# Kernel tuning notes

Hardware: AMD Instinct MI355X
Metric: run time of the kernel (lower is better)

The kernel has to match this reference:

```python
import jax, jax.numpy as jnp
import numpy as np

NEG = -1e30  # log-space 'zero' that keeps gradients finite (vs -inf)


def setup_inputs() -> dict:
    key = jax.random.key(0)
    k1, k2, k3, k4 = jax.random.split(key, 4)
    B, T, V, S = 32, 2048, 128, 256
    predictions = jax.random.normal(k1, (B, T, V), dtype=jnp.float32)
    # input lengths in [T//2, T]; target lengths in [S//4, S]; labels in [1, V) (0 is blank)
    prediction_lengths = jax.random.randint(k2, (B,), T // 2, T + 1, dtype=jnp.int32)
    ground_truths = jax.random.randint(k3, (B, S), 1, V, dtype=jnp.int32)
    ground_truth_lengths = jax.random.randint(k4, (B,), S // 4, S + 1, dtype=jnp.int32)
    return {
        "predictions": predictions,
        "prediction_lengths": prediction_lengths,
        "ground_truths": ground_truths,
        "ground_truth_lengths": ground_truth_lengths,
    }


def _ctc_loss(log_probs, targets, input_lengths, target_lengths, blank=0):
    # log_probs: [T, B, V]; targets: [B, S]
    T, B, V = log_probs.shape
    S = targets.shape[1]
    L = 2 * S + 1  # extended label sequence: blank, l1, blank, l2, ..., blank
    ext = jnp.full((B, L), blank, dtype=targets.dtype).at[:, 1::2].set(targets)
    # skip transition s-2 -> s allowed iff ext[s] != blank and ext[s] != ext[s-2]
    skip = jnp.concatenate(
        [jnp.zeros((B, 2), dtype=bool), (ext[:, 2:] != blank) & (ext[:, 2:] != ext[:, :-2])],
        axis=1,
    )
    # gather per-extended-label log-probs: [T, B, L]
    lp_ext = jnp.take_along_axis(log_probs, jnp.broadcast_to(ext[None], (T, B, L)), axis=2)

    alpha0 = (
        jnp.full((B, L), NEG, dtype=log_probs.dtype)
        .at[:, 0].set(lp_ext[0, :, 0])
        .at[:, 1].set(lp_ext[0, :, 1])
    )

    def step(alpha, lp_t):
        a1 = alpha
        a2 = jnp.pad(alpha[:, :-1], ((0, 0), (1, 0)), constant_values=NEG)
        a3 = jnp.where(skip, jnp.pad(alpha[:, :-2], ((0, 0), (2, 0)), constant_values=NEG), NEG)
        m = jnp.maximum(jnp.maximum(a1, a2), a3)
        new = m + jnp.log(jnp.exp(a1 - m) + jnp.exp(a2 - m) + jnp.exp(a3 - m)) + lp_t
        return new, new

    _, alphas = jax.lax.scan(step, alpha0, lp_ext[1:])
    alphas = jnp.concatenate([alpha0[None], alphas], axis=0)  # [T, B, L]

    bidx = jnp.arange(B)
    alpha_final = alphas[input_lengths - 1, bidx]  # [B, L] at each sequence's last frame
    last = 2 * target_lengths  # index of final blank; last-1 is final label
    loss = -jnp.logaddexp(alpha_final[bidx, last], alpha_final[bidx, last - 1])
    loss = jnp.where(loss < 1e10, loss, 0.0)  # zero_infinity=True
    # torch reduction='mean': per-sample loss / target_length, then batch mean
    return (loss / target_lengths.astype(loss.dtype)).mean()


def reference(predictions, prediction_lengths, ground_truths, ground_truth_lengths):
    # module: transpose to [T, B, V], log_softmax over vocab, then CTC loss
    log_probs = jax.nn.log_softmax(jnp.transpose(predictions, (1, 0, 2)), axis=2)
    return _ctc_loss(log_probs, ground_truths, prediction_lengths, ground_truth_lengths, blank=0)
```

## Files before the change

kernel.cpp:

```cpp
#include <hip/hip_runtime.h>
#include <math.h>

constexpr int V = 128;

__device__ __forceinline__ double dpp_shr1_f64(double x) {
    int lo = __builtin_amdgcn_update_dpp(0, __double2loint(x), 0x138, 0xf, 0xf, false);
    int hi = __builtin_amdgcn_update_dpp(0, __double2hiint(x), 0x138, 0xf, 0xf, false);
    return __hiloint2double(hi, lo);
}
__device__ __forceinline__ double dpp_shl1_f64(double x) {
    int lo = __builtin_amdgcn_update_dpp(0, __double2loint(x), 0x130, 0xf, 0xf, false);
    int hi = __builtin_amdgcn_update_dpp(0, __double2hiint(x), 0x130, 0xf, 0xf, false);
    return __hiloint2double(hi, lo);
}

__global__ __launch_bounds__(256) void ctc_prelude(
    const float* __restrict__ pred, const int* __restrict__ gt,
    const int* __restrict__ gt_len, const int* __restrict__ pred_len,
    float* __restrict__ g, float* __restrict__ z, float* __restrict__ x0a,
    int T, int S)
{
    int wid  = blockIdx.x * 4 + (threadIdx.x >> 6);
    int lane = threadIdx.x & 63;
    int w4   = threadIdx.x >> 6;
    int b    = wid / T;
    int t    = wid - b * T;
    if (t >= pred_len[b]) return;
    __shared__ float rows[4][V];

    const float2* p = (const float2*)pred + (size_t)wid * 64;
    float2 v = p[lane];
    rows[w4][2 * lane]     = v.x;
    rows[w4][2 * lane + 1] = v.y;
    float x0 = __shfl(v.x, 0, 64);
    float s = __expf(v.x) + __expf(v.y);
    #pragma unroll
    for (int off = 32; off >= 1; off >>= 1) s += __shfl_xor(s, off, 64);
    if (lane == 0) { z[wid] = __logf(s); x0a[wid] = v.x; }

    int4 la = *(const int4*)(gt + b * S + 4 * lane);
    int tl = gt_len[b];
    float4 o;
    o.x = (4 * lane + 0 < tl) ? __expf(rows[w4][la.x] - x0) : 0.f;
    o.y = (4 * lane + 1 < tl) ? __expf(rows[w4][la.y] - x0) : 0.f;
    o.z = (4 * lane + 2 < tl) ? __expf(rows[w4][la.z] - x0) : 0.f;
    o.w = (4 * lane + 3 < tl) ? __expf(rows[w4][la.w] - x0) : 0.f;
    *(float4*)(g + (size_t)wid * 256 + 4 * lane) = o;
}

__global__ __launch_bounds__(64) void ctc_scan_bi(
    const float* __restrict__ g,
    const int*   __restrict__ pred_len,
    const int*   __restrict__ gt,
    const int*   __restrict__ gt_len,
    const float* __restrict__ z,
    const float* __restrict__ x0a,
    double*      __restrict__ fwdv,
    double*      __restrict__ bwdv,
    int*         __restrict__ Kf,
    int*         __restrict__ Kb,
    int* done, int* gdone, float* lossb,
    float* __restrict__ out,
    int T, int S, int B)
{
    const int blk  = blockIdx.x;
    const int b    = blk >> 1;
    const int dir  = blk & 1;
    const int lane = threadIdx.x;
    const int len  = pred_len[b];
    const int tl   = gt_len[b];
    const int L    = 2 * tl + 1;
    const int m    = (len + 1) >> 1;

    int4 la = *(const int4*)(gt + b * S + 4 * lane);
    int law_up = __shfl_up(la.w, 1, 64);
    int lax_dn = __shfl_down(la.x, 1, 64);
    const double sk0 = (lane > 0 && la.x != law_up) ? 1.0 : 0.0;
    const double sk1 = (la.y != la.x) ? 1.0 : 0.0;
    const double sk2 = (la.z != la.y) ? 1.0 : 0.0;
    const double sk3 = (la.w != la.z) ? 1.0 : 0.0;
    const double sk4 = (lax_dn != la.w) ? 1.0 : 0.0;

    const char* gb = (const char*)(g + (size_t)b * T * 256) + lane * 16;

    float4 raw[16];
    double u[9];
    int K = 0;

    auto RESCALE = [&]() {
        double mx = u[0];
        #pragma unroll
        for (int j = 1; j < 9; ++j) mx = fmax(mx, u[j]);
        #pragma unroll
        for (int off = 32; off >= 1; off >>= 1)
            mx = fmax(mx, __shfl_xor(mx, off, 64));
        int k = ((__double2hiint(mx) >> 20) & 0x7ff) - 1023;
        #pragma unroll
        for (int j = 0; j < 9; ++j) u[j] = ldexp(u[j], -k);
        K += k;
    };

    if (dir == 0) {
        #pragma unroll
        for (int i = 0; i < 16; ++i)
            raw[i] = *(const float4*)(gb + (size_t)i * 1024);
        #pragma unroll
        for (int j = 0; j < 9; ++j) u[j] = 0.0;
        if (lane == 0) { u[0] = 1.0; u[1] = (double)raw[0].x; }
        raw[0] = *(const float4*)(gb + (size_t)16 * 1024);
        const char* pf = gb + (size_t)17 * 1024;

        auto FSTEP = [&](int i) {
            float4 g4 = raw[i];
            raw[i] = *(const float4*)pf; pf += 1024;
            double um1 = dpp_shr1_f64(u[7]);
            double gx = (double)g4.x, gy = (double)g4.y;
            double gz = (double)g4.z, gw = (double)g4.w;
            u[8] = u[8] + u[7];
            u[7] = (fma(sk3, u[5], u[6]) + u[7]) * gw;
            u[6] = u[6] + u[5];
            u[5] = (fma(sk2, u[3], u[4]) + u[5]) * gz;
            u[4] = u[4] + u[3];
            u[3] = (fma(sk1, u[1], u[2]) + u[3]) * gy;
            u[2] = u[2] + u[1];
            u[1] = (fma(sk0, um1, u[0]) + u[1]) * gx;
            u[0] = u[0] + um1;
        };

        #pragma unroll
        for (int t = 1; t < 16; ++t) FSTEP(t);
        int tb = 16;
        for (; tb + 16 <= m; tb += 16) {
            #pragma unroll
            for (int i = 0; i < 16; ++i) FSTEP(i);
            if (((tb + 16) & 63) == 0) RESCALE();
        }
        #pragma unroll
        for (int i = 0; i < 15; ++i)
            if (tb + i < m) FSTEP(i);
        RESCALE();

        double* outv = fwdv + (size_t)b * 520;
        #pragma unroll
        for (int j = 0; j < 8; ++j) outv[8 * lane + j] = u[j];
        if (lane == 63) outv[512] = u[8];
        if (lane == 0)  Kf[b] = K;
    } else {
        const int nb = len - m;
        #pragma unroll
        for (int i = 0; i < 16; ++i)
            raw[i] = *(const float4*)(gb + (size_t)(len - 1 - i) * 1024);
        #pragma unroll
        for (int j = 0; j < 8; ++j) {
            int s = 8 * lane + j;
            u[j] = (s == 2 * tl || s == 2 * tl - 1) ? 1.0 : 0.0;
        }
        u[8] = (L == 513) ? 1.0 : 0.0;
        const char* pf = gb + (size_t)(len - 17) * 1024;

        auto BSTEP = [&](int i) {
            float4 g4 = raw[i];
            raw[i] = *(const float4*)pf; pf -= 1024;
            double d0 = dpp_shl1_f64(u[0]);
            if (lane == 63) d0 = u[8];
            double p1 = (double)g4.x * u[1], p3 = (double)g4.y * u[3];
            double p5 = (double)g4.z * u[5], p7 = (double)g4.w * u[7];
            double dp = dpp_shl1_f64(p1);
            u[0] = u[0] + p1;
            u[1] = fma(sk1, p3, u[2]) + p1;
            u[2] = u[2] + p3;
            u[3] = fma(sk2, p5, u[4]) + p3;
            u[4] = u[4] + p5;
            u[5] = fma(sk3, p7, u[6]) + p5;
            u[6] = u[6] + p7;
            u[7] = fma(sk4, dp, d0) + p7;
        };

        #pragma unroll
        for (int k = 0; k < 16; ++k) BSTEP(k);
        int kb = 16;
        for (; kb + 16 <= nb; kb += 16) {
            #pragma unroll
            for (int i = 0; i < 16; ++i) BSTEP(i);
            if (((kb + 16) & 63) == 0) RESCALE();
        }
        #pragma unroll
        for (int i = 0; i < 15; ++i)
            if (kb + i < nb) BSTEP(i);
        RESCALE();

        double* outv = bwdv + (size_t)b * 520;
        #pragma unroll
        for (int j = 0; j < 8; ++j) outv[8 * lane + j] = u[j];
        if (lane == 63) outv[512] = u[8];
        if (lane == 0)  Kb[b] = K;
    }

    __threadfence();
    int prev = 0;
    if (lane == 0)
        prev = __hip_atomic_fetch_add(&done[b], 1, __ATOMIC_ACQ_REL,
                                      __HIP_MEMORY_SCOPE_AGENT);
    prev = __shfl(prev, 0, 64);
    if (prev == 0) return;
    __threadfence();

    const double* f = fwdv + (size_t)b * 520;
    const double* w = bwdv + (size_t)b * 520;
    double c = 0.0;
    #pragma unroll
    for (int j = 0; j < 8; ++j)
        c = fma(f[8 * lane + j], w[8 * lane + j], c);
    if (lane == 63) c = fma(f[512], w[512], c);
    #pragma unroll
    for (int off = 32; off >= 1; off >>= 1) c += __shfl_xor(c, off, 64);

    double zs = 0.0;
    for (int t = lane; t < len; t += 64)
        zs += (double)z[b * T + t] - (double)x0a[b * T + t];
    #pragma unroll
    for (int off = 32; off >= 1; off >>= 1) zs += __shfl_xor(zs, off, 64);

    if (lane == 0) {
        double logp = log(c)
                    + (double)(Kf[b] + Kb[b]) * 0.6931471805599453 - zs;
        double loss = -logp;
        if (!(loss < 1e10)) loss = 0.0;
        lossb[b] = (float)(loss / (double)tl);
        __threadfence();
        int pg = __hip_atomic_fetch_add(gdone, 1, __ATOMIC_ACQ_REL,
                                        __HIP_MEMORY_SCOPE_AGENT);
        if (pg == B - 1) {
            __threadfence();
            float ssum = 0.0f;
            for (int i = 0; i < B; ++i) ssum += lossb[i];
            out[0] = ssum / (float)B;
        }
    }
}

constexpr int SPL  = 9;
constexpr int RING = 32;

__global__ void ctc_reduce_kernel(const float* __restrict__ ls,
                                  float* __restrict__ out, int B)
{
    if (blockIdx.x == 0 && threadIdx.x == 0) {
        float s = 0.0f;
        for (int i = 0; i < B; ++i) s += ls[i];
        out[0] = s / (float)B;
    }
}

__global__ __launch_bounds__(256) void softmax_z_kernel(
    const float* __restrict__ pred, float* __restrict__ z, int nrows)
{
    int w    = blockIdx.x * 4 + (threadIdx.x >> 6);
    int lane = threadIdx.x & 63;
    if (w >= nrows) return;
    const float2* p = (const float2*)pred;
    float2 v = p[(size_t)w * 64 + lane];
    float s = __expf(v.x) + __expf(v.y);
    #pragma unroll
    for (int off = 32; off >= 1; off >>= 1) s += __shfl_xor(s, off, 64);
    if (lane == 0) z[w] = __logf(s);
}

__device__ __forceinline__ void ctc_step_fb(
    const float* __restrict__ rowbase, const int* __restrict__ goff,
    const double* __restrict__ skd, double (&u)[SPL], int lane)
{
    float gf[SPL];
    #pragma unroll
    for (int j = 0; j < SPL; ++j)
        gf[j] = *(const float*)((const char*)rowbase + goff[j]);
    double um1 = __shfl_up(u[8], 1, 64);
    double um2 = __shfl_up(u[7], 1, 64);
    if (lane == 0) { um1 = 0.0; um2 = 0.0; }
    #pragma unroll
    for (int jj = 0; jj < SPL; ++jj) {
        int j = SPL - 1 - jj;
        double a2 = (j >= 1) ? u[j - 1] : um1;
        double a3 = (j >= 2) ? u[j - 2] : ((j == 1) ? um1 : um2);
        double t  = fma(skd[j], a3, a2) + u[j];
        u[j] = t * (double)gf[j];
    }
}

__device__ __forceinline__ void ctc_rescale_fb(double (&u)[SPL], int& K)
{
    double m = u[0];
    #pragma unroll
    for (int j = 1; j < SPL; ++j) m = fmax(m, u[j]);
    #pragma unroll
    for (int off = 32; off >= 1; off >>= 1) m = fmax(m, __shfl_xor(m, off, 64));
    if (m > 0.0) {
        int e = (__double2hiint(m) >> 20) & 0x7ff;
        int k = e - 1023;
        #pragma unroll
        for (int j = 0; j < SPL; ++j) u[j] = ldexp(u[j], -k);
        K += k;
    }
}

__global__ __launch_bounds__(64) void ctc_scan_kernel(
    const float* __restrict__ pred, const int* __restrict__ pred_len,
    const int* __restrict__ gt, const int* __restrict__ gt_len,
    const float* __restrict__ z, float* __restrict__ loss_out, int T, int S)
{
    const int b    = blockIdx.x;
    const int lane = threadIdx.x;
    const int len  = pred_len[b];
    const int tl   = gt_len[b];
    const int L    = 2 * tl + 1;

    __shared__ float ring[RING][V];
    __shared__ int   gts[512];

    for (int i = lane; i < S; i += 64) gts[i] = gt[b * S + i];
    __syncthreads();

    int    goff[SPL];
    double skd[SPL];
    #pragma unroll
    for (int j = 0; j < SPL; ++j) {
        int s = SPL * lane + j;
        int e = 0, ep = 0;
        if (s < L && (s & 1)) e = gts[s >> 1];
        if (s >= 2 && s < L && (s & 1)) ep = gts[(s - 2) >> 1];
        goff[j] = e * 4;
        skd[j]  = (s >= 2 && s < L && e != 0 && e != ep) ? 1.0 : 0.0;
    }

    const float2* rowp = (const float2*)(pred + (size_t)b * T * V);
    float2 raw[16];

    #pragma unroll
    for (int i = 0; i < 16; ++i) raw[i] = rowp[(size_t)i * 64 + lane];
    #pragma unroll
    for (int i = 0; i < 16; ++i) {
        float2 w; w.x = __expf(raw[i].x); w.y = __expf(raw[i].y);
        *(float2*)&ring[i][2 * lane] = w;
    }
    #pragma unroll
    for (int i = 0; i < 16; ++i) raw[i] = rowp[(size_t)(16 + i) * 64 + lane];
    #pragma unroll
    for (int i = 0; i < 16; ++i) {
        float2 w; w.x = __expf(raw[i].x); w.y = __expf(raw[i].y);
        *(float2*)&ring[16 + i][2 * lane] = w;
    }
    #pragma unroll
    for (int i = 0; i < 16; ++i) {
        int r = 32 + i; if (r > T - 1) r = T - 1;
        raw[i] = rowp[(size_t)r * 64 + lane];
    }

    double u[SPL];
    #pragma unroll
    for (int j = 0; j < SPL; ++j) {
        int s = SPL * lane + j;
        float w0 = *(const float*)((const char*)&ring[0][0] + goff[j]);
        u[j] = (s < 2) ? (double)w0 : 0.0;
    }
    int K = 0;

    for (int t = 1; t < 16 && t < len; ++t)
        ctc_step_fb(&ring[t & (RING - 1)][0], goff, skd, u, lane);
    ctc_rescale_fb(u, K);

    int tb = 16;
    for (; tb + 16 <= len; tb += 16) {
        #pragma unroll
        for (int i = 0; i < 16; ++i) {
            float2 w; w.x = __expf(raw[i].x); w.y = __expf(raw[i].y);
            *(float2*)&ring[(tb + 16 + i) & (RING - 1)][2 * lane] = w;
        }
        #pragma unroll
        for (int i = 0; i < 16; ++i) {
            int r = tb + 32 + i; if (r > T - 1) r = T - 1;
            raw[i] = rowp[(size_t)r * 64 + lane];
        }
        #pragma unroll
        for (int i = 0; i < 16; ++i)
            ctc_step_fb(&ring[(tb + i) & (RING - 1)][0], goff, skd, u, lane);
        ctc_rescale_fb(u, K);
    }

    for (int t = tb; t < len; ++t)
        ctc_step_fb(&ring[t & (RING - 1)][0], goff, skd, u, lane);

    double contrib = 0.0;
    #pragma unroll
    for (int j = 0; j < SPL; ++j) {
        int s = SPL * lane + j;
        if (s == L - 1 || s == L - 2) contrib += u[j];
    }
    #pragma unroll
    for (int off = 32; off >= 1; off >>= 1)
        contrib += __shfl_xor(contrib, off, 64);

    double zsum = 0.0;
    for (int t = lane; t < len; t += 64) zsum += (double)z[b * T + t];
    #pragma unroll
    for (int off = 32; off >= 1; off >>= 1)
        zsum += __shfl_xor(zsum, off, 64);

    if (lane == 0) {
        double lg    = log(contrib);
        double alpha = lg + (double)K * 0.6931471805599453 - zsum;
        double loss  = -alpha;
        if (!(loss < 1e10)) loss = 0.0;
        loss_out[b] = (float)(loss / (double)tl);
    }
}

extern "C" void kernel_launch(void* const* d_in, const int* in_sizes, int n_in,
                              void* d_out, int out_size, void* d_ws, size_t ws_size,
                              hipStream_t stream) {
    const float* pred = (const float*)d_in[0];
    const int*   plen = (const int*)d_in[1];
    const int*   gts  = (const int*)d_in[2];
    const int*   glen = (const int*)d_in[3];

    const int B = in_sizes[1];
    const int S = in_sizes[2] / B;
    const int T = in_sizes[0] / (B * V);
    const size_t BT = (size_t)B * T;

    float* out = (float*)d_out;
    char*  ws  = (char*)d_ws;

    size_t off_fl  = 0;
    size_t off_z   = 1024;
    size_t off_x0  = off_z   + BT * 4;
    size_t off_fw  = (off_x0 + BT * 4 + 255) & ~(size_t)255;
    size_t off_bw  = off_fw  + (size_t)B * 520 * 8;
    size_t off_kf  = off_bw  + (size_t)B * 520 * 8;
    size_t off_kb  = off_kf  + (size_t)B * 4;
    size_t off_g   = (off_kb + (size_t)B * 4 + 1023) & ~(size_t)1023;
    size_t need    = off_g + BT * 256 * 4;

    bool fast_ok = (ws_size >= need) && (S == 256) && (T % 4 == 0) &&
                   (T >= 96) && (B >= 1) && (B <= 64);

    if (fast_ok) {
        int*    done  = (int*)(ws + off_fl);
        int*    gdone = (int*)(ws + off_fl + 256);
        float*  lossb = (float*)(ws + off_fl + 512);
        float*  zp    = (float*)(ws + off_z);
        float*  x0a   = (float*)(ws + off_x0);
        double* fw    = (double*)(ws + off_fw);
        double* bw    = (double*)(ws + off_bw);
        int*    kf    = (int*)(ws + off_kf);
        int*    kb    = (int*)(ws + off_kb);
        float*  g     = (float*)(ws + off_g);

        hipMemsetAsync(ws + off_fl, 0, 512, stream);
        ctc_prelude<<<B * T / 4, 256, 0, stream>>>(pred, gts, glen, plen,
                                                   g, zp, x0a, T, S);
        ctc_scan_bi<<<2 * B, 64, 0, stream>>>(g, plen, gts, glen, zp, x0a,
                                              fw, bw, kf, kb,
                                              done, gdone, lossb, out, T, S, B);
    } else {
        float* zbuf = (float*)ws;
        float* lb   = zbuf + BT;
        int nrows = B * T;
        softmax_z_kernel<<<(nrows + 3) / 4, 256, 0, stream>>>(pred, zbuf, nrows);
        ctc_scan_kernel<<<B, 64, 0, stream>>>(pred, plen, gts, glen, zbuf, lb, T, S);
        ctc_reduce_kernel<<<1, 64, 0, stream>>>(lb, out, B);
    }
}
```

Before: 174.9 us.

## Switch CTC alpha/beta recurrences from fp64 to fp32 with per-lane exponent scaling

Runs the forward and backward CTC scans in fp32 instead of fp64. Because fp32 has too little range for one shared scale, each lane now keeps its own power-of-two exponent, and neighbouring lanes' exponents are kept within 32 of each other by a DPP-based propagation. Values crossing between lanes are adjusted by a factor, rescaling happens every 8 steps, and the final combine merges per-lane exponents in fp64. This aims to cut fp64 ALU and DPP cost on the serial critical path, but adds rescale work and risks accuracy or underflow problems.

```diff
diff --git a/kernel.cpp b/kernel.cpp
--- a/kernel.cpp
+++ b/kernel.cpp
@@ -3,15 +3,19 @@
 
 constexpr int V = 128;
 
-__device__ __forceinline__ double dpp_shr1_f64(double x) {
-    int lo = __builtin_amdgcn_update_dpp(0, __double2loint(x), 0x138, 0xf, 0xf, false);
-    int hi = __builtin_amdgcn_update_dpp(0, __double2hiint(x), 0x138, 0xf, 0xf, false);
-    return __hiloint2double(hi, lo);
-}
-__device__ __forceinline__ double dpp_shl1_f64(double x) {
-    int lo = __builtin_amdgcn_update_dpp(0, __double2loint(x), 0x130, 0xf, 0xf, false);
-    int hi = __builtin_amdgcn_update_dpp(0, __double2hiint(x), 0x130, 0xf, 0xf, false);
-    return __hiloint2double(hi, lo);
+__device__ __forceinline__ float dpp_shr1_f32(float x) {
+    int v = __builtin_amdgcn_update_dpp(0, __float_as_int(x), 0x138, 0xf, 0xf, false);
+    return __int_as_float(v);
+}
+__device__ __forceinline__ float dpp_shl1_f32(float x) {
+    int v = __builtin_amdgcn_update_dpp(0, __float_as_int(x), 0x130, 0xf, 0xf, false);
+    return __int_as_float(v);
+}
+__device__ __forceinline__ int dpp_shr1_i32(int x) {
+    return __builtin_amdgcn_update_dpp(0, x, 0x138, 0xf, 0xf, false);
+}
+__device__ __forceinline__ int dpp_shl1_i32(int x) {
+    return __builtin_amdgcn_update_dpp(0, x, 0x130, 0xf, 0xf, false);
 }
 
 __global__ __launch_bounds__(256) void ctc_prelude(
@@ -55,10 +59,10 @@
     const int*   __restrict__ gt_len,
     const float* __restrict__ z,
     const float* __restrict__ x0a,
-    double*      __restrict__ fwdv,
-    double*      __restrict__ bwdv,
-    int*         __restrict__ Kf,
-    int*         __restrict__ Kb,
+    float*       __restrict__ fwdv,
+    float*       __restrict__ bwdv,
+    int*         __restrict__ Kfv,
+    int*         __restrict__ Kbv,
     int* done, int* gdone, float* lossb,
     float* __restrict__ out,
     int T, int S, int B)
@@ -75,76 +79,99 @@
     int4 la = *(const int4*)(gt + b * S + 4 * lane);
     int law_up = __shfl_up(la.w, 1, 64);
     int lax_dn = __shfl_down(la.x, 1, 64);
-    const double sk0 = (lane > 0 && la.x != law_up) ? 1.0 : 0.0;
-    const double sk1 = (la.y != la.x) ? 1.0 : 0.0;
-    const double sk2 = (la.z != la.y) ? 1.0 : 0.0;
-    const double sk3 = (la.w != la.z) ? 1.0 : 0.0;
-    const double sk4 = (lax_dn != la.w) ? 1.0 : 0.0;
+    const float sk0 = (lane > 0 && la.x != law_up) ? 1.f : 0.f;
+    const float sk1 = (la.y != la.x) ? 1.f : 0.f;
+    const float sk2 = (la.z != la.y) ? 1.f : 0.f;
+    const float sk3 = (la.w != la.z) ? 1.f : 0.f;
+    const float sk4 = (lax_dn != la.w) ? 1.f : 0.f;
 
     const char* gb = (const char*)(g + (size_t)b * T * 256) + lane * 16;
 
     float4 raw[16];
-    double u[9];
-    int K = 0;
-
-    auto RESCALE = [&]() {
-        double mx = u[0];
-        #pragma unroll
-        for (int j = 1; j < 9; ++j) mx = fmax(mx, u[j]);
-        #pragma unroll
-        for (int off = 32; off >= 1; off >>= 1)
-            mx = fmax(mx, __shfl_xor(mx, off, 64));
-        int k = ((__double2hiint(mx) >> 20) & 0x7ff) - 1023;
-        #pragma unroll
-        for (int j = 0; j < 9; ++j) u[j] = ldexp(u[j], -k);
-        K += k;
-    };
+    float u[9];
+    int   K   = 0;
+    float fac = 1.0f;
 
     if (dir == 0) {
         #pragma unroll
         for (int i = 0; i < 16; ++i)
             raw[i] = *(const float4*)(gb + (size_t)i * 1024);
         #pragma unroll
-        for (int j = 0; j < 9; ++j) u[j] = 0.0;
-        if (lane == 0) { u[0] = 1.0; u[1] = (double)raw[0].x; }
+        for (int j = 0; j < 9; ++j) u[j] = 0.f;
+        if (lane == 0) { u[0] = 1.f; u[1] = raw[0].x; }
         raw[0] = *(const float4*)(gb + (size_t)16 * 1024);
         const char* pf = gb + (size_t)17 * 1024;
+
+        auto RESCALE = [&]() {
+            float mx = u[0];
+            #pragma unroll
+            for (int j = 1; j < 9; ++j) mx = fmaxf(mx, u[j]);
+            bool dead = !(mx > 0.f);
+            int  k = dead ? 0 : ((int)((__float_as_uint(mx) >> 23) & 0xff) - 127);
+            #pragma unroll
+            for (int j = 0; j < 9; ++j) u[j] = ldexpf(u[j], -k);
+            K += k;
+            int K0 = K;
+            int nbrdead = dpp_shr1_i32(dead ? 1 : 0);
+            if (lane == 0) nbrdead = 1;
+            int Kn = 0;
+            #pragma unroll
+            for (int r = 0; r < 16; ++r) {
+                Kn = dpp_shr1_i32(K);
+                int cand = Kn - 32;
+                int Kr = (!dead && !nbrdead && cand > K) ? cand : K;
+                K = dead ? Kn : Kr;
+            }
+            int up = K - K0;
+            if (up > 0) {
+                #pragma unroll
+                for (int j = 0; j < 9; ++j) u[j] = ldexpf(u[j], -up);
+            }
+            int d = Kn - K;
+            d = d < -126 ? -126 : (d > 32 ? 32 : d);
+            fac = ldexpf(1.0f, d);
+        };
 
         auto FSTEP = [&](int i) {
             float4 g4 = raw[i];
             raw[i] = *(const float4*)pf; pf += 1024;
-            double um1 = dpp_shr1_f64(u[7]);
-            double gx = (double)g4.x, gy = (double)g4.y;
-            double gz = (double)g4.z, gw = (double)g4.w;
+            float um1 = dpp_shr1_f32(u[7]) * fac;
             u[8] = u[8] + u[7];
-            u[7] = (fma(sk3, u[5], u[6]) + u[7]) * gw;
+            u[7] = (fmaf(sk3, u[5], u[6]) + u[7]) * g4.w;
             u[6] = u[6] + u[5];
-            u[5] = (fma(sk2, u[3], u[4]) + u[5]) * gz;
+            u[5] = (fmaf(sk2, u[3], u[4]) + u[5]) * g4.z;
             u[4] = u[4] + u[3];
-            u[3] = (fma(sk1, u[1], u[2]) + u[3]) * gy;
+            u[3] = (fmaf(sk1, u[1], u[2]) + u[3]) * g4.y;
             u[2] = u[2] + u[1];
-            u[1] = (fma(sk0, um1, u[0]) + u[1]) * gx;
+            u[1] = (fmaf(sk0, um1, u[0]) + u[1]) * g4.x;
             u[0] = u[0] + um1;
         };
 
         #pragma unroll
-        for (int t = 1; t < 16; ++t) FSTEP(t);
+        for (int t = 1; t < 16; ++t) {
+            FSTEP(t);
+            if (t == 7 || t == 15) RESCALE();
+        }
         int tb = 16;
         for (; tb + 16 <= m; tb += 16) {
             #pragma unroll
-            for (int i = 0; i < 16; ++i) FSTEP(i);
-            if (((tb + 16) & 63) == 0) RESCALE();
-        }
-        #pragma unroll
-        for (int i = 0; i < 15; ++i)
+            for (int i = 0; i < 16; ++i) {
+                FSTEP(i);
+                if (i == 7 || i == 15) RESCALE();
+            }
+        }
+        #pragma unroll
+        for (int i = 0; i < 15; ++i) {
             if (tb + i < m) FSTEP(i);
+            if (i == 7) RESCALE();
+        }
         RESCALE();
 
-        double* outv = fwdv + (size_t)b * 520;
+        float* outv = fwdv + (size_t)b * 520;
         #pragma unroll
         for (int j = 0; j < 8; ++j) outv[8 * lane + j] = u[j];
         if (lane == 63) outv[512] = u[8];
-        if (lane == 0)  Kf[b] = K;
+        Kfv[b * 64 + lane] = K;
     } else {
         const int nb = len - m;
         #pragma unroll
@@ -153,47 +180,84 @@
         #pragma unroll
         for (int j = 0; j < 8; ++j) {
             int s = 8 * lane + j;
-            u[j] = (s == 2 * tl || s == 2 * tl - 1) ? 1.0 : 0.0;
-        }
-        u[8] = (L == 513) ? 1.0 : 0.0;
+            u[j] = (s == 2 * tl || s == 2 * tl - 1) ? 1.f : 0.f;
+        }
+        u[8] = (lane == 63 && L == 513) ? 1.f : 0.f;
         const char* pf = gb + (size_t)(len - 17) * 1024;
+
+        auto RESCALE = [&]() {
+            float mx = u[0];
+            #pragma unroll
+            for (int j = 1; j < 9; ++j) mx = fmaxf(mx, u[j]);
+            bool dead = !(mx > 0.f);
+            int  k = dead ? 0 : ((int)((__float_as_uint(mx) >> 23) & 0xff) - 127);
+            #pragma unroll
+            for (int j = 0; j < 9; ++j) u[j] = ldexpf(u[j], -k);
+            K += k;
+            int K0 = K;
+            int nbrdead = dpp_shl1_i32(dead ? 1 : 0);
+            if (lane == 63) nbrdead = 1;
+            int Kn = 0;
+            #pragma unroll
+            for (int r = 0; r < 16; ++r) {
+                Kn = dpp_shl1_i32(K);
+                int cand = Kn - 32;
+                int Kr = (!dead && !nbrdead && cand > K) ? cand : K;
+                K = dead ? Kn : Kr;
+            }
+            int up = K - K0;
+            if (up > 0) {
+                #pragma unroll
+                for (int j = 0; j < 9; ++j) u[j] = ldexpf(u[j], -up);
+            }
+            int d = Kn - K;
+            d = d < -126 ? -126 : (d > 32 ? 32 : d);
+            fac = ldexpf(1.0f, d);
+        };
 
         auto BSTEP = [&](int i) {
             float4 g4 = raw[i];
             raw[i] = *(const float4*)pf; pf -= 1024;
-            double d0 = dpp_shl1_f64(u[0]);
+            float d0 = dpp_shl1_f32(u[0]) * fac;
             if (lane == 63) d0 = u[8];
-            double p1 = (double)g4.x * u[1], p3 = (double)g4.y * u[3];
-            double p5 = (double)g4.z * u[5], p7 = (double)g4.w * u[7];
-            double dp = dpp_shl1_f64(p1);
+            float p1 = g4.x * u[1], p3 = g4.y * u[3];
+            float p5 = g4.z * u[5], p7 = g4.w * u[7];
+            float dp = dpp_shl1_f32(p1) * fac;
             u[0] = u[0] + p1;
-            u[1] = fma(sk1, p3, u[2]) + p1;
+            u[1] = fmaf(sk1, p3, u[2]) + p1;
             u[2] = u[2] + p3;
-            u[3] = fma(sk2, p5, u[4]) + p3;
+            u[3] = fmaf(sk2, p5, u[4]) + p3;
             u[4] = u[4] + p5;
-            u[5] = fma(sk3, p7, u[6]) + p5;
+            u[5] = fmaf(sk3, p7, u[6]) + p5;
             u[6] = u[6] + p7;
-            u[7] = fma(sk4, dp, d0) + p7;
+            u[7] = fmaf(sk4, dp, d0) + p7;
         };
 
         #pragma unroll
-        for (int k = 0; k < 16; ++k) BSTEP(k);
+        for (int k = 0; k < 16; ++k) {
+            BSTEP(k);
+            if (k == 7 || k == 15) RESCALE();
+        }
         int kb = 16;
         for (; kb + 16 <= nb; kb += 16) {
             #pragma unroll
-            for (int i = 0; i < 16; ++i) BSTEP(i);
-            if (((kb + 16) & 63) == 0) RESCALE();
-        }
-        #pragma unroll
-        for (int i = 0; i < 15; ++i)
+            for (int i = 0; i < 16; ++i) {
+                BSTEP(i);
+                if (i == 7 || i == 15) RESCALE();
+            }
+        }
+        #pragma unroll
+        for (int i = 0; i < 15; ++i) {
             if (kb + i < nb) BSTEP(i);
+            if (i == 7) RESCALE();
+        }
         RESCALE();
 
-        double* outv = bwdv + (size_t)b * 520;
+        float* outv = bwdv + (size_t)b * 520;
         #pragma unroll
         for (int j = 0; j < 8; ++j) outv[8 * lane + j] = u[j];
         if (lane == 63) outv[512] = u[8];
-        if (lane == 0)  Kb[b] = K;
+        Kbv[b * 64 + lane] = K;
     }
 
     __threadfence();
@@ -205,15 +269,24 @@
     if (prev == 0) return;
     __threadfence();
 
-    const double* f = fwdv + (size_t)b * 520;
-    const double* w = bwdv + (size_t)b * 520;
+    const float* f = fwdv + (size_t)b * 520;
+    const float* w = bwdv + (size_t)b * 520;
     double c = 0.0;
     #pragma unroll
     for (int j = 0; j < 8; ++j)
-        c = fma(f[8 * lane + j], w[8 * lane + j], c);
-    if (lane == 63) c = fma(f[512], w[512], c);
-    #pragma unroll
-    for (int off = 32; off >= 1; off >>= 1) c += __shfl_xor(c, off, 64);
+        c = fma((double)f[8 * lane + j], (double)w[8 * lane + j], c);
+    if (lane == 63) c = fma((double)f[512], (double)w[512], c);
+
+    int E = Kfv[b * 64 + lane] + Kbv[b * 64 + lane];
+    int Ee = (c > 0.0) ? E : (int)0xC0000000;
+    #pragma unroll
+    for (int off = 32; off >= 1; off >>= 1) {
+        int o = __shfl_xor(Ee, off, 64);
+        Ee = Ee > o ? Ee : o;
+    }
+    double cs = (c > 0.0) ? ldexp(c, E - Ee) : 0.0;
+    #pragma unroll
+    for (int off = 32; off >= 1; off >>= 1) cs += __shfl_xor(cs, off, 64);
 
     double zs = 0.0;
     for (int t = lane; t < len; t += 64)
@@ -222,10 +295,11 @@
     for (int off = 32; off >= 1; off >>= 1) zs += __shfl_xor(zs, off, 64);
 
     if (lane == 0) {
-        double logp = log(c)
-                    + (double)(Kf[b] + Kb[b]) * 0.6931471805599453 - zs;
+        double logp = log(cs)
+                    + (double)Ee * 0.6931471805599453 - zs;
         double loss = -logp;
         if (!(loss < 1e10)) loss = 0.0;
+        if (loss < 0.0)     loss = 0.0;
         lossb[b] = (float)(loss / (double)tl);
         __threadfence();
         int pg = __hip_atomic_fetch_add(gdone, 1, __ATOMIC_ACQ_REL,
@@ -434,10 +508,10 @@
     size_t off_z   = 1024;
     size_t off_x0  = off_z   + BT * 4;
     size_t off_fw  = (off_x0 + BT * 4 + 255) & ~(size_t)255;
-    size_t off_bw  = off_fw  + (size_t)B * 520 * 8;
-    size_t off_kf  = off_bw  + (size_t)B * 520 * 8;
-    size_t off_kb  = off_kf  + (size_t)B * 4;
-    size_t off_g   = (off_kb + (size_t)B * 4 + 1023) & ~(size_t)1023;
+    size_t off_bw  = off_fw  + (size_t)B * 520 * 4;
+    size_t off_kf  = off_bw  + (size_t)B * 520 * 4;
+    size_t off_kb  = off_kf  + (size_t)B * 64 * 4;
+    size_t off_g   = (off_kb + (size_t)B * 64 * 4 + 1023) & ~(size_t)1023;
     size_t need    = off_g + BT * 256 * 4;
 
     bool fast_ok = (ws_size >= need) && (S == 256) && (T % 4 == 0) &&
@@ -449,8 +523,8 @@
         float*  lossb = (float*)(ws + off_fl + 512);
         float*  zp    = (float*)(ws + off_z);
         float*  x0a   = (float*)(ws + off_x0);
-        double* fw    = (double*)(ws + off_fw);
-        double* bw    = (double*)(ws + off_bw);
+        float*  fw    = (float*)(ws + off_fw);
+        float*  bw    = (float*)(ws + off_bw);
         int*    kf    = (int*)(ws + off_kf);
         int*    kb    = (int*)(ws + off_kb);
         float*  g     = (float*)(ws + off_g);
```

Result: slower. 193.1 us (+10.4%).
